# Performance work log

Measured on AMD Instinct MI355X. Metric: run time of the kernel, lower is better.

The kernel has to match this reference:

```python
import jax, jax.numpy as jnp
import numpy as np

N_PATCHES = 262144
N_BAGS = 32
INPUT_DIM = 1024
FEAT_DIM = 256
ATTN_DIM = 128
HEAD_DIM = 2


def setup_inputs() -> dict:
    key = jax.random.key(0)
    ks = jax.random.split(key, 9)
    s = 0.02
    return {
        "features": jax.random.normal(ks[0], (N_PATCHES, INPUT_DIM), jnp.float32),
        "W1": jax.random.normal(ks[1], (FEAT_DIM, INPUT_DIM), jnp.float32) * s,
        "b1": jnp.zeros((FEAT_DIM,), jnp.float32),
        "Wa1": jax.random.normal(ks[2], (ATTN_DIM, FEAT_DIM), jnp.float32) * s,
        "ba1": jnp.zeros((ATTN_DIM,), jnp.float32),
        "Wa2": jax.random.normal(ks[3], (1, ATTN_DIM), jnp.float32) * s,
        "ba2": jnp.zeros((1,), jnp.float32),
        "Wh": jax.random.normal(ks[4], (HEAD_DIM, FEAT_DIM), jnp.float32) * s,
        "bh": jnp.zeros((HEAD_DIM,), jnp.float32),
        "bag_sizes": jnp.full((N_BAGS,), N_PATCHES // N_BAGS, jnp.int32),
    }


def reference(features, W1, b1, Wa1, ba1, Wa2, ba2, Wh, bh, bag_sizes):
    # encoder: Linear(input_dim -> features_dim) + ReLU
    h = jax.nn.relu(features @ W1.T + b1)                        # [N, F]
    # attention MLP: Linear -> tanh -> Linear -> scalar score
    a = jnp.tanh(h @ Wa1.T + ba1)                                # [N, A]
    scores = (a @ Wa2.T + ba2)[:, 0]                             # [N]
    # segmented softmax over bags + attention-weighted reduce
    seg = jnp.repeat(jnp.arange(N_BAGS), bag_sizes, total_repeat_length=N_PATCHES)
    m = jax.ops.segment_max(scores, seg, num_segments=N_BAGS)    # [B]
    e = jnp.exp(scores - m[seg])                                 # [N]
    z = jax.ops.segment_sum(e, seg, num_segments=N_BAGS)         # [B]
    attn = e / z[seg]                                            # [N]
    bag_emb = jax.ops.segment_sum(attn[:, None] * h, seg, num_segments=N_BAGS)  # [B, F]
    # linear head
    return bag_emb @ Wh.T + bh                                   # [B, head_dim]
```

## Files before the change

### kernel.cpp

```cpp
#include <hip/hip_runtime.h>
#include <cstdint>
#include <cstddef>

typedef short short8 __attribute__((ext_vector_type(8)));
typedef float f32x4 __attribute__((ext_vector_type(4)));
typedef int   i32x4 __attribute__((ext_vector_type(4)));

#define NPATCH 262144
#define NBAGS  32
#define IN_DIM 1024
#define F_DIM  256
#define A_DIM  128
#define ROWSB  128
#define NBLK   (NPATCH / ROWSB)

__device__ __forceinline__ unsigned short f2bf(float f){
  uint32_t u = __builtin_bit_cast(uint32_t, f);
  u += 0x7fffu + ((u >> 16) & 1u);
  return (unsigned short)(u >> 16);
}
__device__ __forceinline__ float bf2f(unsigned short h){
  return __builtin_bit_cast(float, (uint32_t)h << 16);
}
__device__ __forceinline__ float tanh_fast(float x){
  float e = __expf(2.f * x);
  return (e - 1.f) * __builtin_amdgcn_rcpf(e + 1.f);
}
__device__ __forceinline__ uint32_t cvtpk(float a, float b){
  uint32_t r;
  asm("v_cvt_pk_bf16_f32 %0, %1, %2" : "=v"(r) : "v"(a), "v"(b));
  return r;
}
__device__ __forceinline__ void gload_lds16(const void* g, void* l){
  __builtin_amdgcn_global_load_lds((const __attribute__((address_space(1))) void*)g,
                                   (__attribute__((address_space(3))) void*)l, 16, 0, 0);
}

#define MFMA(a,b,c) __builtin_amdgcn_mfma_f32_16x16x32_bf16((a),(b),(c),0,0,0)
#define SWZH(r) (((r) & 7) << 4)

__global__ void prep_kernel(const float* __restrict__ W1, const float* __restrict__ Wa1,
                            unsigned short* __restrict__ w1b, unsigned short* __restrict__ wa1b,
                            float* __restrict__ bagAcc){
  int id = blockIdx.x * 256 + threadIdx.x;
  if (id < F_DIM*IN_DIM) {
    w1b[id] = f2bf(W1[id]);
  } else if (id < F_DIM*IN_DIM + A_DIM*F_DIM) {
    int j = id - F_DIM*IN_DIM;
    wa1b[j] = f2bf(Wa1[j]);
  } else if (id < F_DIM*IN_DIM + A_DIM*F_DIM + NBAGS*257) {
    bagAcc[id - (F_DIM*IN_DIM + A_DIM*F_DIM)] = 0.f;
  }
}

__global__ __launch_bounds__(512, 4)
void mil_main(const float* __restrict__ feat,
              const unsigned short* __restrict__ w1b,
              const float* __restrict__ b1,
              const unsigned short* __restrict__ wa1b,
              const float* __restrict__ ba1,
              const float* __restrict__ wa2,
              const float* __restrict__ ba2v,
              float* __restrict__ bagAcc)
{
  extern __shared__ char lds[];
  char* Bt0 = lds;
  char* Bt1 = lds + 32768;
  char* HsB = lds;
  float* sc8  = (float*)(lds + 65536);
  float* evec = (float*)(lds + 65536 + 4096);
  float* Pp   = (float*)(lds + 65536 + 4096 + 512);

  const int tid  = threadIdx.x;
  const int wid  = tid >> 6;
  const int lane = tid & 63;
  const int l15  = lane & 15;
  const int l4   = lane >> 4;
  const int bRow = blockIdx.x * ROWSB;
  const int wRow = wid * 16;

  const float* aG = feat + (size_t)(bRow + wRow + l15) * IN_DIM + l4*8;

  const char* srcB;
  {
    int D0 = wid*4096 + lane*16;
    int c0 = D0 >> 7, k0 = D0 & 127;
    srcB = (const char*)w1b + (size_t)c0*2048 + (k0 ^ ((c0 & 7) << 4));
  }

#define STAGEB(bb, g) do { \
    _Pragma("unroll") \
    for (int i_ = 0; i_ < 4; ++i_) \
      gload_lds16(srcB + (size_t)i_*16384 + (size_t)(g)*128, \
                  (bb) + wid*4096 + i_*1024); \
  } while(0)

#define LOADA(R, t) do { \
    const float* p_ = aG + (t)*32; \
    R[0] = *(const float4*)p_;  R[1] = *(const float4*)(p_ + 4); \
  } while(0)

#define AFRAG(af, R) do { \
    const float* v_ = (const float*)(R); \
    i32x4 w_ = { (int)cvtpk(v_[0], v_[1]), (int)cvtpk(v_[2], v_[3]), \
                 (int)cvtpk(v_[4], v_[5]), (int)cvtpk(v_[6], v_[7]) }; \
    af = __builtin_bit_cast(short8, w_); \
  } while(0)

  f32x4 acc[16];
  #pragma unroll
  for (int j = 0; j < 16; ++j) acc[j] = (f32x4){0.f, 0.f, 0.f, 0.f};

  float4 aR0[2], aR1[2];

  STAGEB(Bt0, 0);
  LOADA(aR0, 0);
  LOADA(aR1, 1);
  asm volatile("s_waitcnt vmcnt(4)" ::: "memory");
  __builtin_amdgcn_sched_barrier(0);
  __builtin_amdgcn_s_barrier();

  const int swzk = (l15 & 7) << 4;
  const int rb   = l15 * 128;

  for (int g = 0; g < 16; ++g){
    const char* bb = (g & 1) ? Bt1 : Bt0;
    char*       bn = (g & 1) ? Bt0 : Bt1;
    if (g < 15) STAGEB(bn, g + 1);
    __builtin_amdgcn_sched_barrier(0);

    #pragma unroll
    for (int s = 0; s < 2; ++s){
      short8 af;
      if (s == 0){
        AFRAG(af, aR0);
        if (g < 15) LOADA(aR0, 2*g + 2);
      } else {
        AFRAG(af, aR1);
        if (g < 15) LOADA(aR1, 2*g + 3);
      }
      __builtin_amdgcn_sched_barrier(0);
      const int off = rb + ((s*64 + l4*16) ^ swzk);
      #pragma unroll
      for (int nf = 0; nf < 16; ++nf){
        short8 bf = *(const short8*)(bb + nf*2048 + off);
        acc[nf] = MFMA(af, bf, acc[nf]);
      }
    }
    asm volatile("s_waitcnt vmcnt(4) lgkmcnt(0)" ::: "memory");
    __builtin_amdgcn_sched_barrier(0);
    __builtin_amdgcn_s_barrier();
  }
  __syncthreads();

#undef STAGEB
#undef LOADA
#undef AFRAG

  #pragma unroll
  for (int nf = 0; nf < 16; ++nf){
    float b1v = b1[nf*16 + l15];
    #pragma unroll
    for (int r = 0; r < 4; ++r){
      int row = wRow + l4*4 + r;
      int col = nf*16 + l15;
      float v = fmaxf(acc[nf][r] + b1v, 0.f);
      int by = (row*512 + col*2) ^ SWZH(row);
      *(unsigned short*)(HsB + by) = f2bf(v);
    }
  }
  __syncthreads();

  {
    const int acol = wid*16 + l15;
    f32x4 acc2[8];
    #pragma unroll
    for (int i = 0; i < 8; ++i) acc2[i] = (f32x4){0.f, 0.f, 0.f, 0.f};

    #pragma unroll
    for (int ks2 = 0; ks2 < 8; ++ks2){
      short8 wf = *(const short8*)(const void*)(wa1b + acol*256 + ks2*32 + l4*8);
      #pragma unroll
      for (int mf = 0; mf < 8; ++mf){
        int row = mf*16 + l15;
        int by  = (row*512 + (ks2*32 + l4*8)*2) ^ SWZH(row);
        short8 hf = *(const short8*)(HsB + by);
        acc2[mf] = MFMA(hf, wf, acc2[mf]);
      }
    }

    const float ba1v = ba1[acol];
    const float wa2v = wa2[acol];
    #pragma unroll
    for (int mf = 0; mf < 8; ++mf)
      #pragma unroll
      for (int r = 0; r < 4; ++r){
        float p = tanh_fast(acc2[mf][r] + ba1v) * wa2v;
        p += __shfl_xor(p, 1);
        p += __shfl_xor(p, 2);
        p += __shfl_xor(p, 4);
        p += __shfl_xor(p, 8);
        if (l15 == 0){
          int row = mf*16 + l4*4 + r;
          sc8[row*8 + wid] = p;
        }
      }
  }
  __syncthreads();

  if (tid < 128){
    float s = sc8[tid*8+0] + sc8[tid*8+1] + sc8[tid*8+2] + sc8[tid*8+3]
            + sc8[tid*8+4] + sc8[tid*8+5] + sc8[tid*8+6] + sc8[tid*8+7] + ba2v[0];
    evec[tid] = __expf(s);
  }
  __syncthreads();

  {
    const int f0 = (tid & 127) << 1;
    const int g  = tid >> 7;
    float p0 = 0.f, p1 = 0.f;
    const int rbase = g << 5;
    #pragma unroll 8
    for (int i = 0; i < 32; ++i){
      const int r = rbase + i;
      const uint32_t hw = *(const uint32_t*)(HsB + ((r*512 + f0*2) ^ SWZH(r)));
      const float e = evec[r];
      p0 = fmaf(e, bf2f((unsigned short)(hw & 0xffffu)), p0);
      p1 = fmaf(e, bf2f((unsigned short)(hw >> 16)),     p1);
    }
    Pp[(g << 8) + f0]     = p0;
    Pp[(g << 8) + f0 + 1] = p1;
  }
  __syncthreads();

  const int bag = bRow >> 13;
  if (tid < 256){
    float s = Pp[tid] + Pp[256 + tid] + Pp[512 + tid] + Pp[768 + tid];
    atomicAdd(&bagAcc[bag*257 + tid], s);
  }
  if (tid < 64){
    float se = evec[tid] + evec[tid + 64];
    se += __shfl_xor(se, 1);
    se += __shfl_xor(se, 2);
    se += __shfl_xor(se, 4);
    se += __shfl_xor(se, 8);
    se += __shfl_xor(se, 16);
    se += __shfl_xor(se, 32);
    if (tid == 0) atomicAdd(&bagAcc[bag*257 + 256], se);
  }
}

__global__ void head_kernel(const float* __restrict__ bagAcc,
                            const float* __restrict__ wh,
                            const float* __restrict__ bh,
                            float* __restrict__ out){
  int t = threadIdx.x;
  int b = t >> 1, d = t & 1;
  const float* P = bagAcc + b*257;
  float invE = 1.f / P[256];
  float acc = 0.f;
  for (int f = 0; f < 256; ++f) acc += P[f] * wh[d*256 + f];
  out[b*2 + d] = acc * invE + bh[d];
}

extern "C" void kernel_launch(void* const* d_in, const int* in_sizes, int n_in,
                              void* d_out, int out_size, void* d_ws, size_t ws_size,
                              hipStream_t stream){
  const float* feat = (const float*)d_in[0];
  const float* W1   = (const float*)d_in[1];
  const float* b1   = (const float*)d_in[2];
  const float* Wa1  = (const float*)d_in[3];
  const float* ba1  = (const float*)d_in[4];
  const float* Wa2  = (const float*)d_in[5];
  const float* ba2  = (const float*)d_in[6];
  const float* Wh   = (const float*)d_in[7];
  const float* bh   = (const float*)d_in[8];

  unsigned short* w1b  = (unsigned short*)d_ws;
  unsigned short* wa1b = (unsigned short*)((char*)d_ws + 524288);
  float* bagAcc        = (float*)((char*)d_ws + 589824);

  prep_kernel<<<1185, 256, 0, stream>>>(W1, Wa1, w1b, wa1b, bagAcc);

  const size_t ldsBytes = 65536 + 4096 + 512 + 4096;
  mil_main<<<NBLK, 512, ldsBytes, stream>>>(feat, w1b, b1, wa1b, ba1,
                                            Wa2, ba2, bagAcc);

  head_kernel<<<1, 64, 0, stream>>>(bagAcc, Wh, bh, (float*)d_out);
}
```

Baseline: 291.9 us.

## Double block rows to 256 with 1024 threads sharing each staged W1 tile

```diff
diff --git a/kernel.cpp b/kernel.cpp
--- a/kernel.cpp
+++ b/kernel.cpp
@@ -11,7 +11,7 @@
 #define IN_DIM 1024
 #define F_DIM  256
 #define A_DIM  128
-#define ROWSB  128
+#define ROWSB  256
 #define NBLK   (NPATCH / ROWSB)
 
 __device__ __forceinline__ unsigned short f2bf(float f){
@@ -53,7 +53,7 @@
   }
 }
 
-__global__ __launch_bounds__(512, 4)
+__global__ __launch_bounds__(1024, 4)
 void mil_main(const float* __restrict__ feat,
               const unsigned short* __restrict__ w1b,
               const float* __restrict__ b1,
@@ -81,18 +81,13 @@
 
   const float* aG = feat + (size_t)(bRow + wRow + l15) * IN_DIM + l4*8;
 
-  const char* srcB;
-  {
-    int D0 = wid*4096 + lane*16;
-    int c0 = D0 >> 7, k0 = D0 & 127;
-    srcB = (const char*)w1b + (size_t)c0*2048 + (k0 ^ ((c0 & 7) << 4));
-  }
+  const char* srcB = (const char*)w1b
+      + (size_t)(wid*8 + (lane >> 3)) * 2048
+      + (((lane & 7) * 16) ^ (((lane >> 3) & 7) << 4));
 
 #define STAGEB(bb, g) do { \
-    _Pragma("unroll") \
-    for (int i_ = 0; i_ < 4; ++i_) \
-      gload_lds16(srcB + (size_t)i_*16384 + (size_t)(g)*128, \
-                  (bb) + wid*4096 + i_*1024); \
+    gload_lds16(srcB +          (size_t)(g)*128, (bb) + wid*1024); \
+    gload_lds16(srcB + 262144 + (size_t)(g)*128, (bb) + wid*1024 + 16384); \
   } while(0)
 
 #define LOADA(R, t) do { \
@@ -157,96 +152,106 @@
 #undef LOADA
 #undef AFRAG
 
-  #pragma unroll
-  for (int nf = 0; nf < 16; ++nf){
-    float b1v = b1[nf*16 + l15];
-    #pragma unroll
-    for (int r = 0; r < 4; ++r){
-      int row = wRow + l4*4 + r;
-      int col = nf*16 + l15;
-      float v = fmaxf(acc[nf][r] + b1v, 0.f);
-      int by = (row*512 + col*2) ^ SWZH(row);
-      *(unsigned short*)(HsB + by) = f2bf(v);
-    }
-  }
-  __syncthreads();
-
-  {
-    const int acol = wid*16 + l15;
-    f32x4 acc2[8];
-    #pragma unroll
-    for (int i = 0; i < 8; ++i) acc2[i] = (f32x4){0.f, 0.f, 0.f, 0.f};
-
-    #pragma unroll
-    for (int ks2 = 0; ks2 < 8; ++ks2){
-      short8 wf = *(const short8*)(const void*)(wa1b + acol*256 + ks2*32 + l4*8);
-      #pragma unroll
-      for (int mf = 0; mf < 8; ++mf){
-        int row = mf*16 + l15;
-        int by  = (row*512 + (ks2*32 + l4*8)*2) ^ SWZH(row);
-        short8 hf = *(const short8*)(HsB + by);
-        acc2[mf] = MFMA(hf, wf, acc2[mf]);
-      }
-    }
-
-    const float ba1v = ba1[acol];
-    const float wa2v = wa2[acol];
-    #pragma unroll
-    for (int mf = 0; mf < 8; ++mf)
-      #pragma unroll
-      for (int r = 0; r < 4; ++r){
-        float p = tanh_fast(acc2[mf][r] + ba1v) * wa2v;
-        p += __shfl_xor(p, 1);
-        p += __shfl_xor(p, 2);
-        p += __shfl_xor(p, 4);
-        p += __shfl_xor(p, 8);
-        if (l15 == 0){
-          int row = mf*16 + l4*4 + r;
-          sc8[row*8 + wid] = p;
+  const int bag = bRow >> 13;
+  for (int hh = 0; hh < 2; ++hh){
+    if ((wid >> 3) == hh){
+      #pragma unroll
+      for (int nf = 0; nf < 16; ++nf){
+        float b1v = b1[nf*16 + l15];
+        #pragma unroll
+        for (int r = 0; r < 4; ++r){
+          int lr  = (wid & 7)*16 + l4*4 + r;
+          int col = nf*16 + l15;
+          float v = fmaxf(acc[nf][r] + b1v, 0.f);
+          int by = (lr*512 + col*2) ^ SWZH(lr);
+          *(unsigned short*)(HsB + by) = f2bf(v);
         }
       }
-  }
-  __syncthreads();
-
-  if (tid < 128){
-    float s = sc8[tid*8+0] + sc8[tid*8+1] + sc8[tid*8+2] + sc8[tid*8+3]
-            + sc8[tid*8+4] + sc8[tid*8+5] + sc8[tid*8+6] + sc8[tid*8+7] + ba2v[0];
-    evec[tid] = __expf(s);
-  }
-  __syncthreads();
-
-  {
-    const int f0 = (tid & 127) << 1;
-    const int g  = tid >> 7;
-    float p0 = 0.f, p1 = 0.f;
-    const int rbase = g << 5;
-    #pragma unroll 8
-    for (int i = 0; i < 32; ++i){
-      const int r = rbase + i;
-      const uint32_t hw = *(const uint32_t*)(HsB + ((r*512 + f0*2) ^ SWZH(r)));
-      const float e = evec[r];
-      p0 = fmaf(e, bf2f((unsigned short)(hw & 0xffffu)), p0);
-      p1 = fmaf(e, bf2f((unsigned short)(hw >> 16)),     p1);
-    }
-    Pp[(g << 8) + f0]     = p0;
-    Pp[(g << 8) + f0 + 1] = p1;
-  }
-  __syncthreads();
-
-  const int bag = bRow >> 13;
-  if (tid < 256){
-    float s = Pp[tid] + Pp[256 + tid] + Pp[512 + tid] + Pp[768 + tid];
-    atomicAdd(&bagAcc[bag*257 + tid], s);
-  }
-  if (tid < 64){
-    float se = evec[tid] + evec[tid + 64];
-    se += __shfl_xor(se, 1);
-    se += __shfl_xor(se, 2);
-    se += __shfl_xor(se, 4);
-    se += __shfl_xor(se, 8);
-    se += __shfl_xor(se, 16);
-    se += __shfl_xor(se, 32);
-    if (tid == 0) atomicAdd(&bagAcc[bag*257 + 256], se);
+    }
+    __syncthreads();
+
+    {
+      const int a8   = wid & 7;
+      const int rh   = wid >> 3;
+      const int acol = a8*16 + l15;
+      f32x4 acc2[4];
+      #pragma unroll
+      for (int i = 0; i < 4; ++i) acc2[i] = (f32x4){0.f, 0.f, 0.f, 0.f};
+
+      #pragma unroll
+      for (int ks2 = 0; ks2 < 8; ++ks2){
+        short8 wf = *(const short8*)(const void*)(wa1b + acol*256 + ks2*32 + l4*8);
+        #pragma unroll
+        for (int mf = 0; mf < 4; ++mf){
+          int lr = rh*64 + mf*16 + l15;
+          int by = (lr*512 + (ks2*32 + l4*8)*2) ^ SWZH(lr);
+          short8 hf = *(const short8*)(HsB + by);
+          acc2[mf] = MFMA(hf, wf, acc2[mf]);
+        }
+      }
+
+      const float ba1v = ba1[acol];
+      const float wa2v = wa2[acol];
+      #pragma unroll
+      for (int mf = 0; mf < 4; ++mf)
+        #pragma unroll
+        for (int r = 0; r < 4; ++r){
+          float p = tanh_fast(acc2[mf][r] + ba1v) * wa2v;
+          p += __shfl_xor(p, 1);
+          p += __shfl_xor(p, 2);
+          p += __shfl_xor(p, 4);
+          p += __shfl_xor(p, 8);
+          if (l15 == 0){
+            int lr = rh*64 + mf*16 + l4*4 + r;
+            sc8[lr*8 + a8] = p;
+          }
+        }
+    }
+    __syncthreads();
+
+    if (tid < 128){
+      float s = sc8[tid*8+0] + sc8[tid*8+1] + sc8[tid*8+2] + sc8[tid*8+3]
+              + sc8[tid*8+4] + sc8[tid*8+5] + sc8[tid*8+6] + sc8[tid*8+7]
+              + ba2v[0];
+      evec[tid] = __expf(s);
+    }
+    __syncthreads();
+
+    {
+      const int f0 = (tid & 127) << 1;
+      const int g  = tid >> 7;
+      float p0 = 0.f, p1 = 0.f;
+      const int rbase = g << 4;
+      #pragma unroll 8
+      for (int i = 0; i < 16; ++i){
+        const int r = rbase + i;
+        const uint32_t hw = *(const uint32_t*)(HsB + ((r*512 + f0*2) ^ SWZH(r)));
+        const float e = evec[r];
+        p0 = fmaf(e, bf2f((unsigned short)(hw & 0xffffu)), p0);
+        p1 = fmaf(e, bf2f((unsigned short)(hw >> 16)),     p1);
+      }
+      Pp[(g << 8) + f0]     = p0;
+      Pp[(g << 8) + f0 + 1] = p1;
+    }
+    __syncthreads();
+
+    if (tid < 256){
+      float s = 0.f;
+      #pragma unroll
+      for (int g = 0; g < 8; ++g) s += Pp[(g << 8) + tid];
+      atomicAdd(&bagAcc[bag*257 + tid], s);
+    }
+    if (tid < 64){
+      float se = evec[tid] + evec[tid + 64];
+      se += __shfl_xor(se, 1);
+      se += __shfl_xor(se, 2);
+      se += __shfl_xor(se, 4);
+      se += __shfl_xor(se, 8);
+      se += __shfl_xor(se, 16);
+      se += __shfl_xor(se, 32);
+      if (tid == 0) atomicAdd(&bagAcc[bag*257 + 256], se);
+    }
+    __syncthreads();
   }
 }
 
@@ -280,11 +285,14 @@
   unsigned short* wa1b = (unsigned short*)((char*)d_ws + 524288);
   float* bagAcc        = (float*)((char*)d_ws + 589824);
 
+  const size_t ldsBytes = 65536 + 4096 + 512 + 8192;
+  hipFuncSetAttribute((const void*)mil_main,
+                      hipFuncAttributeMaxDynamicSharedMemorySize, (int)ldsBytes);
+
   prep_kernel<<<1185, 256, 0, stream>>>(W1, Wa1, w1b, wa1b, bagAcc);
 
-  const size_t ldsBytes = 65536 + 4096 + 512 + 4096;
-  mil_main<<<NBLK, 512, ldsBytes, stream>>>(feat, w1b, b1, wa1b, ba1,
-                                            Wa2, ba2, bagAcc);
+  mil_main<<<NBLK, 1024, ldsBytes, stream>>>(feat, w1b, b1, wa1b, ba1,
+                                             Wa2, ba2, bagAcc);
 
   head_kernel<<<1, 64, 0, stream>>>(bagAcc, Wh, bh, (float*)d_out);
 }
```

New measurement: 668.2 us. 129% more time.

## Double rows per block so each W1 tile feeds two MFMA row fragments

Applied to the files above, without the earlier changes.

```diff
diff --git a/kernel.cpp b/kernel.cpp
--- a/kernel.cpp
+++ b/kernel.cpp
@@ -11,7 +11,7 @@
 #define IN_DIM 1024
 #define F_DIM  256
 #define A_DIM  128
-#define ROWSB  128
+#define ROWSB  256
 #define NBLK   (NPATCH / ROWSB)
 
 __device__ __forceinline__ unsigned short f2bf(float f){
@@ -53,7 +53,7 @@
   }
 }
 
-__global__ __launch_bounds__(512, 4)
+__global__ __launch_bounds__(512, 1)
 void mil_main(const float* __restrict__ feat,
               const unsigned short* __restrict__ w1b,
               const float* __restrict__ b1,
@@ -77,16 +77,14 @@
   const int l15  = lane & 15;
   const int l4   = lane >> 4;
   const int bRow = blockIdx.x * ROWSB;
-  const int wRow = wid * 16;
-
-  const float* aG = feat + (size_t)(bRow + wRow + l15) * IN_DIM + l4*8;
-
-  const char* srcB;
-  {
-    int D0 = wid*4096 + lane*16;
-    int c0 = D0 >> 7, k0 = D0 & 127;
-    srcB = (const char*)w1b + (size_t)c0*2048 + (k0 ^ ((c0 & 7) << 4));
-  }
+  const int wRow = wid * 32;
+
+  const float* aG0 = feat + (size_t)(bRow + wRow + l15) * IN_DIM + l4*8;
+  const float* aG1 = aG0 + (size_t)16 * IN_DIM;
+
+  const char* srcB = (const char*)w1b
+      + (size_t)(wid*32 + (lane >> 3)) * 2048
+      + (((lane & 7) * 16) ^ (((lane >> 3) & 7) << 4));
 
 #define STAGEB(bb, g) do { \
     _Pragma("unroll") \
@@ -96,27 +94,34 @@
   } while(0)
 
 #define LOADA(R, t) do { \
-    const float* p_ = aG + (t)*32; \
-    R[0] = *(const float4*)p_;  R[1] = *(const float4*)(p_ + 4); \
+    const float* p0_ = aG0 + (t)*32; \
+    const float* p1_ = aG1 + (t)*32; \
+    R[0] = *(const float4*)p0_;  R[1] = *(const float4*)(p0_ + 4); \
+    R[2] = *(const float4*)p1_;  R[3] = *(const float4*)(p1_ + 4); \
   } while(0)
 
-#define AFRAG(af, R) do { \
+#define AFRAG2(a0, a1, R) do { \
     const float* v_ = (const float*)(R); \
-    i32x4 w_ = { (int)cvtpk(v_[0], v_[1]), (int)cvtpk(v_[2], v_[3]), \
-                 (int)cvtpk(v_[4], v_[5]), (int)cvtpk(v_[6], v_[7]) }; \
-    af = __builtin_bit_cast(short8, w_); \
+    i32x4 w0_ = { (int)cvtpk(v_[0],  v_[1]),  (int)cvtpk(v_[2],  v_[3]), \
+                  (int)cvtpk(v_[4],  v_[5]),  (int)cvtpk(v_[6],  v_[7]) }; \
+    i32x4 w1_ = { (int)cvtpk(v_[8],  v_[9]),  (int)cvtpk(v_[10], v_[11]), \
+                  (int)cvtpk(v_[12], v_[13]), (int)cvtpk(v_[14], v_[15]) }; \
+    a0 = __builtin_bit_cast(short8, w0_); \
+    a1 = __builtin_bit_cast(short8, w1_); \
   } while(0)
 
-  f32x4 acc[16];
+  f32x4 acc[2][16];
   #pragma unroll
-  for (int j = 0; j < 16; ++j) acc[j] = (f32x4){0.f, 0.f, 0.f, 0.f};
-
-  float4 aR0[2], aR1[2];
+  for (int i = 0; i < 2; ++i)
+    #pragma unroll
+    for (int j = 0; j < 16; ++j) acc[i][j] = (f32x4){0.f, 0.f, 0.f, 0.f};
+
+  float4 aR0[4], aR1[4];
 
   STAGEB(Bt0, 0);
   LOADA(aR0, 0);
   LOADA(aR1, 1);
-  asm volatile("s_waitcnt vmcnt(4)" ::: "memory");
+  asm volatile("s_waitcnt vmcnt(8)" ::: "memory");
   __builtin_amdgcn_sched_barrier(0);
   __builtin_amdgcn_s_barrier();
 
@@ -131,12 +136,12 @@
 
     #pragma unroll
     for (int s = 0; s < 2; ++s){
-      short8 af;
+      short8 af0, af1;
       if (s == 0){
-        AFRAG(af, aR0);
+        AFRAG2(af0, af1, aR0);
         if (g < 15) LOADA(aR0, 2*g + 2);
       } else {
-        AFRAG(af, aR1);
+        AFRAG2(af0, af1, aR1);
         if (g < 15) LOADA(aR1, 2*g + 3);
       }
       __builtin_amdgcn_sched_barrier(0);
@@ -144,10 +149,11 @@
       #pragma unroll
       for (int nf = 0; nf < 16; ++nf){
         short8 bf = *(const short8*)(bb + nf*2048 + off);
-        acc[nf] = MFMA(af, bf, acc[nf]);
-      }
-    }
-    asm volatile("s_waitcnt vmcnt(4) lgkmcnt(0)" ::: "memory");
+        acc[0][nf] = MFMA(af0, bf, acc[0][nf]);
+        acc[1][nf] = MFMA(af1, bf, acc[1][nf]);
+      }
+    }
+    asm volatile("s_waitcnt vmcnt(8) lgkmcnt(0)" ::: "memory");
     __builtin_amdgcn_sched_barrier(0);
     __builtin_amdgcn_s_barrier();
   }
@@ -155,98 +161,106 @@
 
 #undef STAGEB
 #undef LOADA
-#undef AFRAG
-
-  #pragma unroll
-  for (int nf = 0; nf < 16; ++nf){
-    float b1v = b1[nf*16 + l15];
-    #pragma unroll
-    for (int r = 0; r < 4; ++r){
-      int row = wRow + l4*4 + r;
-      int col = nf*16 + l15;
-      float v = fmaxf(acc[nf][r] + b1v, 0.f);
-      int by = (row*512 + col*2) ^ SWZH(row);
-      *(unsigned short*)(HsB + by) = f2bf(v);
-    }
-  }
-  __syncthreads();
-
-  {
-    const int acol = wid*16 + l15;
-    f32x4 acc2[8];
-    #pragma unroll
-    for (int i = 0; i < 8; ++i) acc2[i] = (f32x4){0.f, 0.f, 0.f, 0.f};
-
-    #pragma unroll
-    for (int ks2 = 0; ks2 < 8; ++ks2){
-      short8 wf = *(const short8*)(const void*)(wa1b + acol*256 + ks2*32 + l4*8);
-      #pragma unroll
-      for (int mf = 0; mf < 8; ++mf){
-        int row = mf*16 + l15;
-        int by  = (row*512 + (ks2*32 + l4*8)*2) ^ SWZH(row);
-        short8 hf = *(const short8*)(HsB + by);
-        acc2[mf] = MFMA(hf, wf, acc2[mf]);
-      }
-    }
-
-    const float ba1v = ba1[acol];
-    const float wa2v = wa2[acol];
-    #pragma unroll
-    for (int mf = 0; mf < 8; ++mf)
-      #pragma unroll
-      for (int r = 0; r < 4; ++r){
-        float p = tanh_fast(acc2[mf][r] + ba1v) * wa2v;
-        p += __shfl_xor(p, 1);
-        p += __shfl_xor(p, 2);
-        p += __shfl_xor(p, 4);
-        p += __shfl_xor(p, 8);
-        if (l15 == 0){
-          int row = mf*16 + l4*4 + r;
-          sc8[row*8 + wid] = p;
+#undef AFRAG2
+
+  const int bag = bRow >> 13;
+  for (int hh = 0; hh < 2; ++hh){
+    if ((wid >> 2) == hh){
+      #pragma unroll
+      for (int nf = 0; nf < 16; ++nf){
+        float b1v = b1[nf*16 + l15];
+        #pragma unroll
+        for (int mf = 0; mf < 2; ++mf)
+          #pragma unroll
+          for (int r = 0; r < 4; ++r){
+            int lr  = (wid & 3)*32 + mf*16 + l4*4 + r;
+            int col = nf*16 + l15;
+            float v = fmaxf(acc[mf][nf][r] + b1v, 0.f);
+            int by = (lr*512 + col*2) ^ SWZH(lr);
+            *(unsigned short*)(HsB + by) = f2bf(v);
+          }
+      }
+    }
+    __syncthreads();
+
+    {
+      const int acol = wid*16 + l15;
+      f32x4 acc2[8];
+      #pragma unroll
+      for (int i = 0; i < 8; ++i) acc2[i] = (f32x4){0.f, 0.f, 0.f, 0.f};
+
+      #pragma unroll
+      for (int ks2 = 0; ks2 < 8; ++ks2){
+        short8 wf = *(const short8*)(const void*)(wa1b + acol*256 + ks2*32 + l4*8);
+        #pragma unroll
+        for (int mf = 0; mf < 8; ++mf){
+          int lr = mf*16 + l15;
+          int by = (lr*512 + (ks2*32 + l4*8)*2) ^ SWZH(lr);
+          short8 hf = *(const short8*)(HsB + by);
+          acc2[mf] = MFMA(hf, wf, acc2[mf]);
         }
       }
-  }
-  __syncthreads();
-
-  if (tid < 128){
-    float s = sc8[tid*8+0] + sc8[tid*8+1] + sc8[tid*8+2] + sc8[tid*8+3]
-            + sc8[tid*8+4] + sc8[tid*8+5] + sc8[tid*8+6] + sc8[tid*8+7] + ba2v[0];
-    evec[tid] = __expf(s);
-  }
-  __syncthreads();
-
-  {
-    const int f0 = (tid & 127) << 1;
-    const int g  = tid >> 7;
-    float p0 = 0.f, p1 = 0.f;
-    const int rbase = g << 5;
-    #pragma unroll 8
-    for (int i = 0; i < 32; ++i){
-      const int r = rbase + i;
-      const uint32_t hw = *(const uint32_t*)(HsB + ((r*512 + f0*2) ^ SWZH(r)));
-      const float e = evec[r];
-      p0 = fmaf(e, bf2f((unsigned short)(hw & 0xffffu)), p0);
-      p1 = fmaf(e, bf2f((unsigned short)(hw >> 16)),     p1);
-    }
-    Pp[(g << 8) + f0]     = p0;
-    Pp[(g << 8) + f0 + 1] = p1;
-  }
-  __syncthreads();
-
-  const int bag = bRow >> 13;
-  if (tid < 256){
-    float s = Pp[tid] + Pp[256 + tid] + Pp[512 + tid] + Pp[768 + tid];
-    atomicAdd(&bagAcc[bag*257 + tid], s);
-  }
-  if (tid < 64){
-    float se = evec[tid] + evec[tid + 64];
-    se += __shfl_xor(se, 1);
-    se += __shfl_xor(se, 2);
-    se += __shfl_xor(se, 4);
-    se += __shfl_xor(se, 8);
-    se += __shfl_xor(se, 16);
-    se += __shfl_xor(se, 32);
-    if (tid == 0) atomicAdd(&bagAcc[bag*257 + 256], se);
+
+      const float ba1v = ba1[acol];
+      const float wa2v = wa2[acol];
+      #pragma unroll
+      for (int mf = 0; mf < 8; ++mf)
+        #pragma unroll
+        for (int r = 0; r < 4; ++r){
+          float p = tanh_fast(acc2[mf][r] + ba1v) * wa2v;
+          p += __shfl_xor(p, 1);
+          p += __shfl_xor(p, 2);
+          p += __shfl_xor(p, 4);
+          p += __shfl_xor(p, 8);
+          if (l15 == 0){
+            int lr = mf*16 + l4*4 + r;
+            sc8[lr*8 + wid] = p;
+          }
+        }
+    }
+    __syncthreads();
+
+    if (tid < 128){
+      float s = sc8[tid*8+0] + sc8[tid*8+1] + sc8[tid*8+2] + sc8[tid*8+3]
+              + sc8[tid*8+4] + sc8[tid*8+5] + sc8[tid*8+6] + sc8[tid*8+7]
+              + ba2v[0];
+      evec[tid] = __expf(s);
+    }
+    __syncthreads();
+
+    {
+      const int f0 = (tid & 127) << 1;
+      const int g  = tid >> 7;
+      float p0 = 0.f, p1 = 0.f;
+      const int rbase = g << 5;
+      #pragma unroll 8
+      for (int i = 0; i < 32; ++i){
+        const int r = rbase + i;
+        const uint32_t hw = *(const uint32_t*)(HsB + ((r*512 + f0*2) ^ SWZH(r)));
+        const float e = evec[r];
+        p0 = fmaf(e, bf2f((unsigned short)(hw & 0xffffu)), p0);
+        p1 = fmaf(e, bf2f((unsigned short)(hw >> 16)),     p1);
+      }
+      Pp[(g << 8) + f0]     = p0;
+      Pp[(g << 8) + f0 + 1] = p1;
+    }
+    __syncthreads();
+
+    if (tid < 256){
+      float s = Pp[tid] + Pp[256 + tid] + Pp[512 + tid] + Pp[768 + tid];
+      atomicAdd(&bagAcc[bag*257 + tid], s);
+    }
+    if (tid < 64){
+      float se = evec[tid] + evec[tid + 64];
+      se += __shfl_xor(se, 1);
+      se += __shfl_xor(se, 2);
+      se += __shfl_xor(se, 4);
+      se += __shfl_xor(se, 8);
+      se += __shfl_xor(se, 16);
+      se += __shfl_xor(se, 32);
+      if (tid == 0) atomicAdd(&bagAcc[bag*257 + 256], se);
+    }
+    __syncthreads();
   }
 }
 
@@ -280,9 +294,12 @@
   unsigned short* wa1b = (unsigned short*)((char*)d_ws + 524288);
   float* bagAcc        = (float*)((char*)d_ws + 589824);
 
+  const size_t ldsBytes = 65536 + 4096 + 512 + 4096;
+  hipFuncSetAttribute((const void*)mil_main,
+                      hipFuncAttributeMaxDynamicSharedMemorySize, (int)ldsBytes);
+
   prep_kernel<<<1185, 256, 0, stream>>>(W1, Wa1, w1b, wa1b, bagAcc);
 
-  const size_t ldsBytes = 65536 + 4096 + 512 + 4096;
   mil_main<<<NBLK, 512, ldsBytes, stream>>>(feat, w1b, b1, wa1b, ba1,
                                             Wa2, ba2, bagAcc);
 
```

Result: slower. 827.6 us (+183.5%).
